# Kernel tuning notes

Hardware: AMD Instinct MI355X
Metric: run time of the kernel (lower is better)

Reference implementation:

```python
import jax, jax.numpy as jnp
import numpy as np
import math

L, H, P = 16384, 128, 256


def setup_inputs() -> dict:
    key = jax.random.key(0)
    k = jax.random.split(key, 6)
    return {
        "input_sequence": jax.random.normal(k[0], (L, H), dtype=jnp.float32),
        "A_diag": jax.random.uniform(k[1], (P,), dtype=jnp.float32),
        "B": (jax.random.uniform(k[2], (P, H, 2), dtype=jnp.float32) * 2.0 - 1.0) / math.sqrt(H),
        "C": (jax.random.uniform(k[3], (H, P, 2), dtype=jnp.float32) * 2.0 - 1.0) / math.sqrt(P),
        "D": jax.random.normal(k[4], (H,), dtype=jnp.float32),
        "steps": jax.random.uniform(k[5], (P,), dtype=jnp.float32),
    }


def _binop(qi, qj):
    # 2x2 block-diagonal matrix product + affine state propagation, per channel.
    iA, iB, iC, iD, ib1, ib2 = qi
    jA, jB, jC, jD, jb1, jb2 = qj
    return (
        jA * iA + jB * iC,
        jA * iB + jB * iD,
        jC * iA + jD * iC,
        jC * iB + jD * iD,
        jA * ib1 + jB * ib2 + jb1,
        jC * ib1 + jD * ib2 + jb2,
    )


def reference(input_sequence, A_diag, B, C, D, steps):
    # LinOSS-IM discretization (implicit)
    A = jax.nn.relu(A_diag)                      # (P,)
    dt = jax.nn.sigmoid(steps)                   # (P,)
    Bc = B[..., 0] + 1j * B[..., 1]              # (P,H) complex64
    Cc = C[..., 0] + 1j * C[..., 1]              # (H,P) complex64

    Bu = input_sequence @ Bc.T                   # (L,P) complex64

    schur = 1.0 / (1.0 + dt ** 2 * A)
    M11 = 1.0 - dt ** 2 * A * schur
    M12 = -dt * A * schur
    M21 = dt * schur
    M22 = schur

    ones = jnp.ones((input_sequence.shape[0], A.shape[0]), dtype=input_sequence.dtype)
    F1 = M11 * Bu * dt                           # (L,P) complex
    F2 = M21 * Bu * dt

    elems = (M11 * ones, M12 * ones, M21 * ones, M22 * ones, F1, F2)
    _, _, _, _, _, x2 = jax.lax.associative_scan(_binop, elems)  # scan over L

    ys = jnp.real(x2 @ Cc.T)                     # (L,H)
    return ys + input_sequence * D
```

## Files before the change

kernel.cpp:

```cpp
#include <hip/hip_runtime.h>
#include <math.h>

#define L 16384
#define H 128
#define P 256
#define CL 32
#define NCH (L/CL)
#define GS 16
#define NG (NCH/GS)
#define KDIM 512
#define NBU 512

typedef __attribute__((ext_vector_type(8))) short short8;
typedef __attribute__((ext_vector_type(4))) float f32x4;

__device__ inline unsigned short f2bf(float f){
  union { float f; unsigned u; } v; v.f = f;
  unsigned u = v.u;
  u += 0x7fffu + ((u >> 16) & 1u);
  return (unsigned short)(u >> 16);
}
__device__ inline float bf2f(unsigned short s){
  union { unsigned u; float f; } v; v.u = ((unsigned)s) << 16;
  return v.f;
}

struct Params { float M11,M12,M21,M22,s1,s2; };

__device__ inline Params get_params(const float* A_diag, const float* steps, int p){
  float A = A_diag[p]; A = A > 0.f ? A : 0.f;
  float dt = 1.f/(1.f + expf(-steps[p]));
  float schur = 1.f/(1.f + dt*dt*A);
  Params q;
  q.M11 = 1.f - dt*dt*A*schur;
  q.M12 = -dt*A*schur;
  q.M21 = dt*schur;
  q.M22 = schur;
  q.s1 = q.M11*dt;
  q.s2 = q.M21*dt;
  return q;
}

__global__ __launch_bounds__(512) void prep_all(const float* __restrict__ in,
                                                const float* __restrict__ B,
                                                const float* __restrict__ Cw,
                                                unsigned short* __restrict__ inb,
                                                unsigned short* __restrict__ BWswz,
                                                unsigned short* __restrict__ Bswz){
  int gid = blockIdx.x*512 + threadIdx.x;
  const float4* g = (const float4*)in;
  float4 a = g[gid*2], b4 = g[gid*2+1];
  union { short8 s; unsigned short u[8]; } o;
  o.u[0]=f2bf(a.x); o.u[1]=f2bf(a.y); o.u[2]=f2bf(a.z); o.u[3]=f2bf(a.w);
  o.u[4]=f2bf(b4.x); o.u[5]=f2bf(b4.y); o.u[6]=f2bf(b4.z); o.u[7]=f2bf(b4.w);
  ((short8*)inb)[gid] = o.s;
  if (gid < H*NBU){
    int k = gid >> 9, n = gid & 511;
    int p = n & 255, c2 = n >> 8;
    float v = B[((size_t)p*H + k)*2 + c2];
    BWswz[((size_t)(k>>3)*NBU + n)*8 + (k&7)] = f2bf(v);
  }
  if (gid < KDIM*H){
    int k = gid >> 7, n = gid & 127;
    float v = (k < P) ? Cw[((size_t)n*P + k)*2]
                      : -Cw[((size_t)n*P + (k-P))*2 + 1];
    Bswz[((size_t)(k>>3)*H + n)*8 + (k&7)] = f2bf(v);
  }
}

__device__ inline void chunk_bu_to_lds(int c, const short* __restrict__ inb,
                                       const short* __restrict__ BWswz,
                                       unsigned short (*sBu)[NBU+8]){
  int tid = threadIdx.x;
  int lane = tid & 63, w = tid >> 6;
  int ml = lane & 15, quad = lane >> 4;
  int mt = w & 1, ng = w >> 1;
  int lm0 = mt*16;
  const short* aptr = inb + (size_t)(c*CL + lm0 + ml)*H + quad*8;
  short8 av[4];
  #pragma unroll
  for (int ks=0; ks<4; ks++) av[ks] = *(const short8*)(aptr + ks*32);
  f32x4 acc[8];
  #pragma unroll
  for (int t=0;t<8;t++) acc[t] = (f32x4){0.f,0.f,0.f,0.f};
  #pragma unroll
  for (int ks=0; ks<4; ks++){
    #pragma unroll
    for (int t=0;t<8;t++){
      int n0 = (ng*8 + t)*16;
      short8 bv = *(const short8*)(BWswz + ((size_t)(ks*4+quad)*NBU + n0 + ml)*8);
      acc[t] = __builtin_amdgcn_mfma_f32_16x16x32_bf16(av[ks], bv, acc[t], 0, 0, 0);
    }
  }
  #pragma unroll
  for (int t=0;t<8;t++){
    int n = (ng*8+t)*16 + ml;
    #pragma unroll
    for (int r=0;r<4;r++)
      sBu[lm0 + quad*4 + r][n] = f2bf(acc[t][r]);
  }
}

__global__ __launch_bounds__(512) void bu_finals(const short* __restrict__ inb,
                                                 const short* __restrict__ BWswz,
                                                 const float* __restrict__ A_diag,
                                                 const float* __restrict__ steps,
                                                 float* __restrict__ finals){
  __shared__ unsigned short sBu[CL][NBU+8];
  int c = blockIdx.x;
  chunk_bu_to_lds(c, inb, BWswz, sBu);
  __syncthreads();
  int tid = threadIdx.x;
  int p = tid & 255, part = tid >> 8;
  Params q = get_params(A_diag, steps, p);
  float x1=0.f, x2=0.f;
  #pragma unroll
  for (int i=0;i<CL;i++){
    float u = bf2f(sBu[i][part*256 + p]);
    float n1 = q.M11*x1 + q.M12*x2 + q.s1*u;
    float n2 = q.M21*x1 + q.M22*x2 + q.s2*u;
    x1 = n1; x2 = n2;
  }
  ((float2*)finals)[(size_t)(part*NCH + c)*P + p] = make_float2(x1,x2);
}

__global__ __launch_bounds__(512) void group_scan(const float* __restrict__ A_diag,
                                                  const float* __restrict__ steps,
                                                  float* zf,
                                                  float* __restrict__ gfin){
  int tid = threadIdx.x;
  int p = tid & (P-1);
  int part = tid >> 8;
  int g = blockIdx.x;
  Params q = get_params(A_diag, steps, p);
  float a=q.M11, b=q.M12, c=q.M21, d=q.M22;
  #pragma unroll
  for (int s=0;s<5;s++){
    float na=a*a+b*c, nb=a*b+b*d, nc=c*a+d*c, nd=c*b+d*d;
    a=na;b=nb;c=nc;d=nd;
  }
  float2* z2 = (float2*)zf;
  float x1=0.f, x2=0.f;
  #pragma unroll
  for (int i=0;i<GS;i++){
    size_t idx = (size_t)(part*NCH + g*GS + i)*P + p;
    float2 f = z2[idx];
    z2[idx] = make_float2(x1,x2);
    float n1 = a*x1 + b*x2 + f.x;
    float n2 = c*x1 + d*x2 + f.y;
    x1=n1; x2=n2;
  }
  ((float2*)gfin)[(size_t)(part*NG + g)*P + p] = make_float2(x1,x2);
}

__global__ __launch_bounds__(512) void fused_out(const short* __restrict__ inb,
                                                 const short* __restrict__ BWswz,
                                                 const short* __restrict__ Bswz,
                                                 const float* __restrict__ A_diag,
                                                 const float* __restrict__ steps,
                                                 const float* __restrict__ zloc,
                                                 const float* __restrict__ gfin,
                                                 const float* __restrict__ Dv,
                                                 const float* __restrict__ in,
                                                 float* __restrict__ out){
  __shared__ unsigned short sX[CL][KDIM+8];
  int c = blockIdx.x;
  chunk_bu_to_lds(c, inb, BWswz, sX);
  __syncthreads();

  int tid = threadIdx.x;
  {
    int p = tid & 255, part = tid >> 8;
    int g = c >> 4, iw = c & (GS-1);
    Params q = get_params(A_diag, steps, p);
    float a=q.M11, b=q.M12, cc=q.M21, dd=q.M22;
    #pragma unroll
    for (int s=0;s<5;s++){
      float na=a*a+b*cc, nb=a*b+b*dd, nc=cc*a+dd*cc, nd=cc*b+dd*dd;
      a=na;b=nb;cc=nc;dd=nd;
    }
    float sa=1.f, sb=0.f, sc=0.f, sd=1.f;
    {
      float wa=a, wb=b, wc=cc, wd=dd;
      #pragma unroll
      for (int bit=0; bit<4; bit++){
        if ((iw>>bit)&1){
          float na = wa*sa + wb*sc, nb = wa*sb + wb*sd;
          float nc = wc*sa + wd*sc, nd = wc*sb + wd*sd;
          sa=na; sb=nb; sc=nc; sd=nd;
        }
        float qa = wa*wa + wb*wc, qb = wa*wb + wb*wd;
        float qc = wc*wa + wd*wc, qd = wc*wb + wd*wd;
        wa=qa; wb=qb; wc=qc; wd=qd;
      }
    }
    float ga=a, gb=b, gc=cc, gd=dd;
    #pragma unroll
    for (int s=0;s<4;s++){
      float na=ga*ga+gb*gc, nb=ga*gb+gb*gd, nc=gc*ga+gd*gc, nd=gc*gb+gd*gd;
      ga=na;gb=nb;gc=nc;gd=nd;
    }
    float y1=0.f, y2=0.f;
    const float2* Z2 = (const float2*)gfin;
    for (int j=0; j<g; j++){
      float2 z = Z2[(size_t)(part*NG + j)*P + p];
      float n1 = ga*y1 + gb*y2 + z.x;
      float n2 = gc*y1 + gd*y2 + z.y;
      y1=n1; y2=n2;
    }
    float2 zc = ((const float2*)zloc)[(size_t)(part*NCH + c)*P + p];
    float x1 = sa*y1 + sb*y2 + zc.x;
    float x2 = sc*y1 + sd*y2 + zc.y;
    #pragma unroll
    for (int i=0;i<CL;i++){
      float u = bf2f(sX[i][part*256 + p]);
      float n1 = q.M11*x1 + q.M12*x2 + q.s1*u;
      float n2 = q.M21*x1 + q.M22*x2 + q.s2*u;
      x1 = n1; x2 = n2;
      sX[i][part*256 + p] = f2bf(x2);
    }
  }
  __syncthreads();

  int lane = tid & 63, w = tid >> 6;
  int ml = lane & 15, quad = lane >> 4;
  int mt = w & 1;
  int ntb = (w >> 1) * 2;
  f32x4 acc[2];
  acc[0] = (f32x4){0.f,0.f,0.f,0.f};
  acc[1] = (f32x4){0.f,0.f,0.f,0.f};
  for (int ks=0; ks<KDIM/32; ks++){
    short8 av = *(const short8*)&sX[mt*16 + ml][ks*32 + quad*8];
    #pragma unroll
    for (int j=0;j<2;j++){
      short8 bv = *(const short8*)(Bswz + ((size_t)(ks*4+quad)*H + (ntb+j)*16 + ml)*8);
      acc[j] = __builtin_amdgcn_mfma_f32_16x16x32_bf16(av, bv, acc[j], 0, 0, 0);
    }
  }
  #pragma unroll
  for (int j=0;j<2;j++){
    int h = (ntb+j)*16 + ml;
    float dv = Dv[h];
    #pragma unroll
    for (int r=0;r<4;r++){
      int l = c*CL + mt*16 + quad*4 + r;
      out[(size_t)l*H + h] = acc[j][r] + in[(size_t)l*H + h]*dv;
    }
  }
}

extern "C" void kernel_launch(void* const* d_in, const int* in_sizes, int n_in,
                              void* d_out, int out_size, void* d_ws, size_t ws_size,
                              hipStream_t stream) {
  const float* in     = (const float*)d_in[0];
  const float* A_diag = (const float*)d_in[1];
  const float* B      = (const float*)d_in[2];
  const float* Cw     = (const float*)d_in[3];
  const float* Dv     = (const float*)d_in[4];
  const float* steps  = (const float*)d_in[5];
  float* out = (float*)d_out;

  unsigned short* inb  = (unsigned short*)d_ws;
  unsigned short* BWswz= inb + (size_t)L*H;
  unsigned short* Bswz = BWswz + (size_t)H*NBU;
  float* finals = (float*)(Bswz + (size_t)KDIM*H);
  float* gfin   = finals + (size_t)2*NCH*P*2;

  prep_all<<<512, 512, 0, stream>>>(in, B, Cw, inb, BWswz, Bswz);
  bu_finals<<<NCH, 512, 0, stream>>>((const short*)inb, (const short*)BWswz,
                                     A_diag, steps, finals);
  group_scan<<<NG, 512, 0, stream>>>(A_diag, steps, finals, gfin);
  fused_out<<<NCH, 512, 0, stream>>>((const short*)inb, (const short*)BWswz,
                                     (const short*)Bswz, A_diag, steps,
                                     finals, gfin, Dv, in, out);
}
```

Baseline: 104.3 us.

## Fuse input bf16 conversion into GEMM and group scan into chunk kernel

Drops the separate bf16 copy of the input sequence: the chunk GEMM now loads fp32 input and converts it to bf16 in registers. The group scan kernel is folded into bu_finals using an atomic counter per group, so the last-arriving block of each group runs that group's sequential scan. This cuts one kernel launch and the write and re-read of the bf16 input, in exchange for twice the input read traffic in the GEMM loads plus threadfence and atomic overhead. The weight prep kernel now also zeroes the counters.

```diff
diff --git a/kernel.cpp b/kernel.cpp
--- a/kernel.cpp
+++ b/kernel.cpp
@@ -41,34 +41,28 @@
   return q;
 }
 
-__global__ __launch_bounds__(512) void prep_all(const float* __restrict__ in,
-                                                const float* __restrict__ B,
-                                                const float* __restrict__ Cw,
-                                                unsigned short* __restrict__ inb,
-                                                unsigned short* __restrict__ BWswz,
-                                                unsigned short* __restrict__ Bswz){
+__global__ __launch_bounds__(512) void prep_w(const float* __restrict__ B,
+                                              const float* __restrict__ Cw,
+                                              unsigned short* __restrict__ BWswz,
+                                              unsigned short* __restrict__ Bswz,
+                                              unsigned* __restrict__ cnt){
   int gid = blockIdx.x*512 + threadIdx.x;
-  const float4* g = (const float4*)in;
-  float4 a = g[gid*2], b4 = g[gid*2+1];
-  union { short8 s; unsigned short u[8]; } o;
-  o.u[0]=f2bf(a.x); o.u[1]=f2bf(a.y); o.u[2]=f2bf(a.z); o.u[3]=f2bf(a.w);
-  o.u[4]=f2bf(b4.x); o.u[5]=f2bf(b4.y); o.u[6]=f2bf(b4.z); o.u[7]=f2bf(b4.w);
-  ((short8*)inb)[gid] = o.s;
   if (gid < H*NBU){
     int k = gid >> 9, n = gid & 511;
     int p = n & 255, c2 = n >> 8;
     float v = B[((size_t)p*H + k)*2 + c2];
     BWswz[((size_t)(k>>3)*NBU + n)*8 + (k&7)] = f2bf(v);
-  }
-  if (gid < KDIM*H){
-    int k = gid >> 7, n = gid & 127;
+  } else {
+    int g2 = gid - H*NBU;
+    int k = g2 >> 7, n = g2 & 127;
     float v = (k < P) ? Cw[((size_t)n*P + k)*2]
                       : -Cw[((size_t)n*P + (k-P))*2 + 1];
     Bswz[((size_t)(k>>3)*H + n)*8 + (k&7)] = f2bf(v);
   }
-}
-
-__device__ inline void chunk_bu_to_lds(int c, const short* __restrict__ inb,
+  if (gid < NG) cnt[gid] = 0u;
+}
+
+__device__ inline void chunk_bu_to_lds(int c, const float* __restrict__ in,
                                        const short* __restrict__ BWswz,
                                        unsigned short (*sBu)[NBU+8]){
   int tid = threadIdx.x;
@@ -76,10 +70,17 @@
   int ml = lane & 15, quad = lane >> 4;
   int mt = w & 1, ng = w >> 1;
   int lm0 = mt*16;
-  const short* aptr = inb + (size_t)(c*CL + lm0 + ml)*H + quad*8;
+  const float* aptr = in + (size_t)(c*CL + lm0 + ml)*H + quad*8;
   short8 av[4];
   #pragma unroll
-  for (int ks=0; ks<4; ks++) av[ks] = *(const short8*)(aptr + ks*32);
+  for (int ks=0; ks<4; ks++){
+    float4 f0 = *(const float4*)(aptr + ks*32);
+    float4 f1 = *(const float4*)(aptr + ks*32 + 4);
+    union { short8 s; unsigned short u[8]; } o;
+    o.u[0]=f2bf(f0.x); o.u[1]=f2bf(f0.y); o.u[2]=f2bf(f0.z); o.u[3]=f2bf(f0.w);
+    o.u[4]=f2bf(f1.x); o.u[5]=f2bf(f1.y); o.u[6]=f2bf(f1.z); o.u[7]=f2bf(f1.w);
+    av[ks] = o.s;
+  }
   f32x4 acc[8];
   #pragma unroll
   for (int t=0;t<8;t++) acc[t] = (f32x4){0.f,0.f,0.f,0.f};
@@ -101,14 +102,17 @@
   }
 }
 
-__global__ __launch_bounds__(512) void bu_finals(const short* __restrict__ inb,
+__global__ __launch_bounds__(512) void bu_finals(const float* __restrict__ in,
                                                  const short* __restrict__ BWswz,
                                                  const float* __restrict__ A_diag,
                                                  const float* __restrict__ steps,
-                                                 float* __restrict__ finals){
+                                                 float* finals,
+                                                 float* __restrict__ gfin,
+                                                 unsigned* __restrict__ cnt){
   __shared__ unsigned short sBu[CL][NBU+8];
+  __shared__ int lastFlag;
   int c = blockIdx.x;
-  chunk_bu_to_lds(c, inb, BWswz, sBu);
+  chunk_bu_to_lds(c, in, BWswz, sBu);
   __syncthreads();
   int tid = threadIdx.x;
   int p = tid & 255, part = tid >> 8;
@@ -122,38 +126,36 @@
     x1 = n1; x2 = n2;
   }
   ((float2*)finals)[(size_t)(part*NCH + c)*P + p] = make_float2(x1,x2);
-}
-
-__global__ __launch_bounds__(512) void group_scan(const float* __restrict__ A_diag,
-                                                  const float* __restrict__ steps,
-                                                  float* zf,
-                                                  float* __restrict__ gfin){
-  int tid = threadIdx.x;
-  int p = tid & (P-1);
-  int part = tid >> 8;
-  int g = blockIdx.x;
-  Params q = get_params(A_diag, steps, p);
-  float a=q.M11, b=q.M12, c=q.M21, d=q.M22;
-  #pragma unroll
-  for (int s=0;s<5;s++){
-    float na=a*a+b*c, nb=a*b+b*d, nc=c*a+d*c, nd=c*b+d*d;
-    a=na;b=nb;c=nc;d=nd;
-  }
-  float2* z2 = (float2*)zf;
-  float x1=0.f, x2=0.f;
-  #pragma unroll
-  for (int i=0;i<GS;i++){
-    size_t idx = (size_t)(part*NCH + g*GS + i)*P + p;
-    float2 f = z2[idx];
-    z2[idx] = make_float2(x1,x2);
-    float n1 = a*x1 + b*x2 + f.x;
-    float n2 = c*x1 + d*x2 + f.y;
-    x1=n1; x2=n2;
-  }
-  ((float2*)gfin)[(size_t)(part*NG + g)*P + p] = make_float2(x1,x2);
-}
-
-__global__ __launch_bounds__(512) void fused_out(const short* __restrict__ inb,
+
+  __threadfence();
+  if (tid == 0)
+    lastFlag = (atomicAdd(&cnt[c >> 4], 1u) == GS - 1u);
+  __syncthreads();
+  if (lastFlag){
+    __threadfence();
+    int g = c >> 4;
+    float a=q.M11, b=q.M12, cc=q.M21, d=q.M22;
+    #pragma unroll
+    for (int s=0;s<5;s++){
+      float na=a*a+b*cc, nb=a*b+b*d, nc=cc*a+d*cc, nd=cc*b+d*d;
+      a=na;b=nb;cc=nc;d=nd;
+    }
+    float2* z2 = (float2*)finals;
+    float y1=0.f, y2=0.f;
+    #pragma unroll
+    for (int i=0;i<GS;i++){
+      size_t idx = (size_t)(part*NCH + g*GS + i)*P + p;
+      float2 f = z2[idx];
+      z2[idx] = make_float2(y1,y2);
+      float n1 = a*y1 + b*y2 + f.x;
+      float n2 = cc*y1 + d*y2 + f.y;
+      y1=n1; y2=n2;
+    }
+    ((float2*)gfin)[(size_t)(part*NG + g)*P + p] = make_float2(y1,y2);
+  }
+}
+
+__global__ __launch_bounds__(512) void fused_out(const float* __restrict__ in,
                                                  const short* __restrict__ BWswz,
                                                  const short* __restrict__ Bswz,
                                                  const float* __restrict__ A_diag,
@@ -161,11 +163,10 @@
                                                  const float* __restrict__ zloc,
                                                  const float* __restrict__ gfin,
                                                  const float* __restrict__ Dv,
-                                                 const float* __restrict__ in,
                                                  float* __restrict__ out){
   __shared__ unsigned short sX[CL][KDIM+8];
   int c = blockIdx.x;
-  chunk_bu_to_lds(c, inb, BWswz, sX);
+  chunk_bu_to_lds(c, in, BWswz, sX);
   __syncthreads();
 
   int tid = threadIdx.x;
@@ -260,17 +261,15 @@
   const float* steps  = (const float*)d_in[5];
   float* out = (float*)d_out;
 
-  unsigned short* inb  = (unsigned short*)d_ws;
-  unsigned short* BWswz= inb + (size_t)L*H;
-  unsigned short* Bswz = BWswz + (size_t)H*NBU;
+  unsigned short* BWswz = (unsigned short*)d_ws;
+  unsigned short* Bswz  = BWswz + (size_t)H*NBU;
   float* finals = (float*)(Bswz + (size_t)KDIM*H);
   float* gfin   = finals + (size_t)2*NCH*P*2;
-
-  prep_all<<<512, 512, 0, stream>>>(in, B, Cw, inb, BWswz, Bswz);
-  bu_finals<<<NCH, 512, 0, stream>>>((const short*)inb, (const short*)BWswz,
-                                     A_diag, steps, finals);
-  group_scan<<<NG, 512, 0, stream>>>(A_diag, steps, finals, gfin);
-  fused_out<<<NCH, 512, 0, stream>>>((const short*)inb, (const short*)BWswz,
-                                     (const short*)Bswz, A_diag, steps,
-                                     finals, gfin, Dv, in, out);
-}
+  unsigned* cnt = (unsigned*)(gfin + (size_t)2*NG*P*2);
+
+  prep_w<<<256, 512, 0, stream>>>(B, Cw, BWswz, Bswz, cnt);
+  bu_finals<<<NCH, 512, 0, stream>>>(in, (const short*)BWswz, A_diag, steps,
+                                     finals, gfin, cnt);
+  fused_out<<<NCH, 512, 0, stream>>>(in, (const short*)BWswz, (const short*)Bswz,
+                                     A_diag, steps, finals, gfin, Dv, out);
+}
```

Result: slower. 203.5 us (+95.1%).
